# Performance work log

Hardware: AMD Instinct MI355X
Metric: run time of the kernel (lower is better)

Reference implementation:

```python
import jax, jax.numpy as jnp
import numpy as np

EPS = 1e-5

def _bn_train(h, gamma, beta):
    # BatchNorm1d in training mode: batch mean and biased variance over batch dim
    mu = jnp.mean(h, axis=0)
    var = jnp.mean((h - mu) ** 2, axis=0)
    return (h - mu) * jax.lax.rsqrt(var + EPS) * gamma + beta

def setup_inputs() -> dict:
    key = jax.random.key(0)
    ks = jax.random.split(key, 12)
    B, IN, H1, H2, NC = 16384, 4096, 256, 128, 12
    x = jax.random.normal(ks[0], (B, 1, 64, 64), dtype=jnp.float32)
    y = jax.random.randint(ks[1], (B,), 0, NC, dtype=jnp.int32)
    s1 = 1.0 / np.sqrt(IN)
    W1 = jax.random.uniform(ks[2], (H1, IN), jnp.float32, -s1, s1)
    b1 = jax.random.uniform(ks[3], (H1,), jnp.float32, -s1, s1)
    g1 = jax.random.normal(ks[4], (H1,), jnp.float32) * 0.1 + 1.0
    be1 = jax.random.normal(ks[5], (H1,), jnp.float32) * 0.1
    s2 = 1.0 / np.sqrt(H1)
    W2 = jax.random.uniform(ks[6], (H2, H1), jnp.float32, -s2, s2)
    b2 = jax.random.uniform(ks[7], (H2,), jnp.float32, -s2, s2)
    g2 = jax.random.normal(ks[8], (H2,), jnp.float32) * 0.1 + 1.0
    be2 = jax.random.normal(ks[9], (H2,), jnp.float32) * 0.1
    s4 = 1.0 / np.sqrt(H2)
    W4 = jax.random.uniform(ks[10], (NC, H2), jnp.float32, -s4, s4)
    b4 = jax.random.uniform(ks[11], (NC,), jnp.float32, -s4, s4)
    return {"x": x, "W1": W1, "b1": b1, "g1": g1, "be1": be1,
            "W2": W2, "b2": b2, "g2": g2, "be2": be2,
            "W4": W4, "b4": b4, "y": y}

def reference(x, W1, b1, g1, be1, W2, b2, g2, be2, W4, b4, y):
    B = x.shape[0]
    h = x.reshape(B, -1)  # [B, 4096]
    # layer 1: binarized linear + BN(train) + hardtanh (dropout p=0 is identity)
    h = h @ jnp.sign(W1).T + jnp.sign(b1)
    h = jnp.clip(_bn_train(h, g1, be1), -1.0, 1.0)
    # layer 2
    h = h @ jnp.sign(W2).T + jnp.sign(b2)
    h = jnp.clip(_bn_train(h, g2, be2), -1.0, 1.0)
    # final float linear
    return h @ W4.T + b4  # [B, 12]
```

## Files before the change

kernel.cpp:

```cpp
#include <hip/hip_runtime.h>
#include <cstddef>

typedef __attribute__((ext_vector_type(8))) short short8;
typedef __attribute__((ext_vector_type(4))) float f4;
typedef __attribute__((ext_vector_type(4))) unsigned int u4;

__device__ __forceinline__ unsigned int f2bf(float f){
  unsigned int u = __float_as_uint(f);
  u += 0x7fffu + ((u >> 16) & 1u);
  return u >> 16;
}
__device__ __forceinline__ float bflo(unsigned int w){ return __uint_as_float((w & 0xFFFFu) << 16); }
__device__ __forceinline__ float bfhi(unsigned int w){ return __uint_as_float(w & 0xFFFF0000u); }
__device__ __forceinline__ float fsign(float x){ return (x > 0.f) ? 1.f : ((x < 0.f) ? -1.f : 0.f); }
__device__ __forceinline__ float hclip(float x){ return fminf(1.f, fmaxf(-1.f, x)); }

#define BARRIER() do { \
    __builtin_amdgcn_sched_barrier(0); \
    asm volatile("s_waitcnt lgkmcnt(0)" ::: "memory"); \
    __builtin_amdgcn_s_barrier(); \
    asm volatile("" ::: "memory"); \
    __builtin_amdgcn_sched_barrier(0); \
  } while(0)

#define VBAR(N) do { \
    __builtin_amdgcn_sched_barrier(0); \
    asm volatile("s_waitcnt vmcnt(" #N ") lgkmcnt(0)" ::: "memory"); \
    __builtin_amdgcn_s_barrier(); \
    asm volatile("" ::: "memory"); \
    __builtin_amdgcn_sched_barrier(0); \
  } while(0)

#define GL16(gp, lp) __builtin_amdgcn_global_load_lds( \
    (const __attribute__((address_space(1))) void*)(gp), \
    (__attribute__((address_space(3))) void*)(lp), 16, 0, 0)

__global__ void prep_sign_k(const float* __restrict__ W1, unsigned short* __restrict__ w1s,
                            const float* __restrict__ W2, unsigned short* __restrict__ w2s){
  int i = (blockIdx.x * blockDim.x + threadIdx.x) * 8;
  const float* w; unsigned short* o; int off;
  if (i < 1048576){ w = W1; o = w1s; off = i; }
  else            { w = W2; o = w2s; off = i - 1048576; if (off >= 32768) return; }
  f4 a = *(const f4*)(w + off);
  f4 b = *(const f4*)(w + off + 4);
  unsigned short s[8];
  #pragma unroll
  for (int j = 0; j < 4; j++) s[j]   = (a[j] > 0.f) ? 0x3F80u : ((a[j] < 0.f) ? 0xBF80u : 0u);
  #pragma unroll
  for (int j = 0; j < 4; j++) s[4+j] = (b[j] > 0.f) ? 0x3F80u : ((b[j] < 0.f) ? 0xBF80u : 0u);
  u4 v;
  v.x = (unsigned)s[0] | ((unsigned)s[1] << 16);
  v.y = (unsigned)s[2] | ((unsigned)s[3] << 16);
  v.z = (unsigned)s[4] | ((unsigned)s[5] << 16);
  v.w = (unsigned)s[6] | ((unsigned)s[7] << 16);
  *(u4*)(o + off) = v;
}

__global__ __launch_bounds__(512, 1) void gemm1_k(
    const float* __restrict__ x, const unsigned short* __restrict__ w1s,
    const float* __restrict__ b1, unsigned short* __restrict__ h1,
    float* __restrict__ part1s, float* __restrict__ part1q)
{
  __shared__ __align__(16) char lds[147456];
  const int tid  = threadIdx.x;
  const int lane = tid & 63;
  const int wid  = tid >> 6;
  const int wm   = wid >> 2;
  const int wn   = wid & 3;
  const int cl   = lane & 15;
  const int g    = lane >> 4;
  const int row0 = blockIdx.x * 64;

  const int aoff_o = tid * 16;
  const int boff_o = tid * 16;

  f4 acc[2][4];
  const f4 z = {0.f, 0.f, 0.f, 0.f};
  #pragma unroll
  for (int i = 0; i < 2; i++)
    #pragma unroll
    for (int j = 0; j < 4; j++) acc[i][j] = z;

  auto stage = [&](int buf, int kstep){
    char* abuf = lds + buf * 16384;
    char* bbuf = lds + 49152 + buf * 32768;
    #pragma unroll
    for (int c = 0; c < 2; c++){
      int o  = c * 8192 + aoff_o;
      int m  = o >> 8;
      int kb = (o & 255) ^ ((m & 7) << 5);
      const char* src = (const char*)x + (size_t)(row0 + m) * 16384 + kstep * 256 + kb;
      GL16(src, abuf + o);
    }
    #pragma unroll
    for (int c = 0; c < 4; c++){
      int o  = c * 8192 + boff_o;
      int n  = o >> 7;
      int kb = (o & 127) ^ ((n & 7) << 4);
      const char* src = (const char*)w1s + (size_t)n * 8192 + kstep * 128 + kb;
      GL16(src, bbuf + o);
    }
  };

  auto compute = [&](int buf){
    const char* abuf = lds + buf * 16384;
    const char* bbuf = lds + 49152 + buf * 32768;
    short8 bf[4][2];
    #pragma unroll
    for (int fn = 0; fn < 4; fn++){
      int n = wn * 64 + fn * 16 + cl;
      #pragma unroll
      for (int ks = 0; ks < 2; ks++){
        int off = (n * 128 + ks * 64 + g * 16) ^ ((n & 7) << 4);
        bf[fn][ks] = *(const short8*)(bbuf + off);
      }
    }
    short8 af[2][2];
    #pragma unroll
    for (int fm = 0; fm < 2; fm++){
      int m = wm * 32 + fm * 16 + cl;
      #pragma unroll
      for (int ks = 0; ks < 2; ks++){
        int off = (m * 256 + ks * 128 + g * 32) ^ ((m & 7) << 5);
        f4 lo = *(const f4*)(abuf + off);
        f4 hi = *(const f4*)(abuf + off + 16);
        u4 pk;
        pk.x = f2bf(lo[0]) | (f2bf(lo[1]) << 16);
        pk.y = f2bf(lo[2]) | (f2bf(lo[3]) << 16);
        pk.z = f2bf(hi[0]) | (f2bf(hi[1]) << 16);
        pk.w = f2bf(hi[2]) | (f2bf(hi[3]) << 16);
        af[fm][ks] = *(short8*)&pk;
      }
    }
    #pragma unroll
    for (int ks = 0; ks < 2; ks++)
      #pragma unroll
      for (int fm = 0; fm < 2; fm++)
        #pragma unroll
        for (int fn = 0; fn < 4; fn++)
          acc[fm][fn] = __builtin_amdgcn_mfma_f32_16x16x32_bf16(af[fm][ks], bf[fn][ks], acc[fm][fn], 0, 0, 0);
  };

  stage(0, 0);
  stage(1, 1);
  VBAR(6);
  int cb = 0;
  for (int k = 0; k < 64; ++k){
    int sb = cb + 2; if (sb >= 3) sb -= 3;
    if (k < 62) stage(sb, k + 2);
    compute(cb);
    if (k < 62)      VBAR(6);
    else if (k < 63) VBAR(0);
    cb = (cb == 2) ? 0 : cb + 1;
  }

  #pragma unroll
  for (int fn = 0; fn < 4; fn++){
    int c = wn * 64 + fn * 16 + cl;
    float sb = fsign(b1[c]);
    float s = 0.f, q = 0.f;
    #pragma unroll
    for (int fm = 0; fm < 2; fm++){
      int rbase = row0 + wm * 32 + fm * 16 + g * 4;
      #pragma unroll
      for (int i = 0; i < 4; i++){
        float v = acc[fm][fn][i] + sb;
        h1[(size_t)(rbase + i) * 256 + c] = (unsigned short)f2bf(v);
        s += v; q += v * v;
      }
    }
    s += __shfl_xor(s, 16, 64); s += __shfl_xor(s, 32, 64);
    q += __shfl_xor(q, 16, 64); q += __shfl_xor(q, 32, 64);
    if (g == 0){
      part1s[c * 512 + blockIdx.x * 2 + wm] = s;
      part1q[c * 512 + blockIdx.x * 2 + wm] = q;
    }
  }
}

template<int COLS, int NBLK>
__global__ __launch_bounds__(64) void params_k(
    const float* __restrict__ ps, const float* __restrict__ pq,
    const float* __restrict__ g, const float* __restrict__ be,
    float* __restrict__ ab){
  int j = blockIdx.x * 64 + threadIdx.x;
  const f4* vs = (const f4*)(ps + (size_t)j * NBLK);
  const f4* vq = (const f4*)(pq + (size_t)j * NBLK);
  f4 s4 = {0,0,0,0}, q4 = {0,0,0,0};
  #pragma unroll 8
  for (int b = 0; b < NBLK/4; b++){ s4 += vs[b]; q4 += vq[b]; }
  float s = s4[0]+s4[1]+s4[2]+s4[3];
  float q = q4[0]+q4[1]+q4[2]+q4[3];
  float mu  = s * (1.f/16384.f);
  float var = q * (1.f/16384.f) - mu*mu;
  float a   = g[j] * rsqrtf(var + 1e-5f);
  ab[j] = a;
  ab[COLS + j] = be[j] - mu*a;
}

__global__ __launch_bounds__(512) void gemm2_k(
    const unsigned short* __restrict__ h1, const unsigned short* __restrict__ w2s,
    const float* __restrict__ b2, const float* __restrict__ ab1,
    unsigned short* __restrict__ h2, float* __restrict__ part2s, float* __restrict__ part2q)
{
  __shared__ __align__(16) char lds[32768];
  __shared__ __align__(16) float a1l[256];
  __shared__ __align__(16) float c1l[256];
  const int tid  = threadIdx.x;
  const int lane = tid & 63;
  const int wid  = tid >> 6;
  const int cl   = lane & 15;
  const int g    = lane >> 4;
  const int klo  = g * 8;
  const int row0 = blockIdx.x * 64;

  if (tid < 256) a1l[tid] = ab1[tid];
  else           c1l[tid - 256] = ab1[tid];

  const int am  = tid >> 3;
  const int ak0 = (tid & 7) * 8;
  const unsigned short* hA = h1 + (size_t)(row0 + am) * 256 + ak0;
  const int aw = ((am * 128) + (ak0 * 2)) ^ ((am & 7) << 4);
  const unsigned short* wbase = w2s + (size_t)(wid * 16 + cl) * 256 + klo;

  u4 q0 = *(const u4*)(hA);
  u4 q1 = *(const u4*)(hA + 64);
  u4 q2 = *(const u4*)(hA + 128);
  u4 q3 = *(const u4*)(hA + 192);
  short8 Bq0, Bq1, Br0, Br1;
  Bq0 = *(const short8*)(wbase);
  Bq1 = *(const short8*)(wbase + 32);

  BARRIER();

#define TRW(KB, RAW) do { \
    f4 _a0 = *(const f4*)(&a1l[(KB)*64 + ak0]); \
    f4 _a1 = *(const f4*)(&a1l[(KB)*64 + ak0 + 4]); \
    f4 _c0 = *(const f4*)(&c1l[(KB)*64 + ak0]); \
    f4 _c1 = *(const f4*)(&c1l[(KB)*64 + ak0 + 4]); \
    float _t0 = hclip(_a0[0]*bflo(RAW.x) + _c0[0]); \
    float _t1 = hclip(_a0[1]*bfhi(RAW.x) + _c0[1]); \
    float _t2 = hclip(_a0[2]*bflo(RAW.y) + _c0[2]); \
    float _t3 = hclip(_a0[3]*bfhi(RAW.y) + _c0[3]); \
    float _t4 = hclip(_a1[0]*bflo(RAW.z) + _c1[0]); \
    float _t5 = hclip(_a1[1]*bfhi(RAW.z) + _c1[1]); \
    float _t6 = hclip(_a1[2]*bflo(RAW.w) + _c1[2]); \
    float _t7 = hclip(_a1[3]*bfhi(RAW.w) + _c1[3]); \
    u4 _v; \
    _v.x = f2bf(_t0) | (f2bf(_t1) << 16); \
    _v.y = f2bf(_t2) | (f2bf(_t3) << 16); \
    _v.z = f2bf(_t4) | (f2bf(_t5) << 16); \
    _v.w = f2bf(_t6) | (f2bf(_t7) << 16); \
    *(u4*)(lds + (KB)*8192 + aw) = _v; \
  } while(0)

  TRW(0, q0); TRW(1, q1); TRW(2, q2); TRW(3, q3);
#undef TRW
  BARRIER();

  f4 acc[4];
  const f4 z = {0.f, 0.f, 0.f, 0.f};
  #pragma unroll
  for (int i = 0; i < 4; i++) acc[i] = z;

#define LOADB2(P, KB) do { \
    B##P##0 = *(const short8*)(wbase + (KB)*64); \
    B##P##1 = *(const short8*)(wbase + (KB)*64 + 32); \
  } while(0)

#define COMP2(BASE, P) do { \
    const char* _ab = (const char*)(BASE); \
    short8 _af[4][2]; \
    _Pragma("unroll") \
    for (int fm = 0; fm < 4; fm++){ \
      int _m = fm*16 + cl; \
      _af[fm][0] = *(const short8*)(_ab + ((_m*128 + klo*2) ^ ((_m & 7) << 4))); \
      _af[fm][1] = *(const short8*)(_ab + ((_m*128 + (32 + klo)*2) ^ ((_m & 7) << 4))); \
    } \
    _Pragma("unroll") \
    for (int fm = 0; fm < 4; fm++){ \
      acc[fm] = __builtin_amdgcn_mfma_f32_16x16x32_bf16(_af[fm][0], B##P##0, acc[fm], 0, 0, 0); \
      acc[fm] = __builtin_amdgcn_mfma_f32_16x16x32_bf16(_af[fm][1], B##P##1, acc[fm], 0, 0, 0); \
    } \
  } while(0)

  LOADB2(r, 1);
  COMP2(lds,         q);
  LOADB2(q, 2);
  COMP2(lds +  8192, r);
  LOADB2(r, 3);
  COMP2(lds + 16384, q);
  COMP2(lds + 24576, r);
#undef COMP2
#undef LOADB2

  {
    int c = wid*16 + cl;
    float sb = fsign(b2[c]);
    float s = 0.f, q = 0.f;
    #pragma unroll
    for (int fm = 0; fm < 4; fm++){
      int rbase = row0 + fm*16 + g*4;
      #pragma unroll
      for (int i = 0; i < 4; i++){
        float v = acc[fm][i] + sb;
        h2[(size_t)(rbase + i)*128 + c] = (unsigned short)f2bf(v);
        s += v; q += v*v;
      }
    }
    s += __shfl_xor(s, 16, 64); s += __shfl_xor(s, 32, 64);
    q += __shfl_xor(q, 16, 64); q += __shfl_xor(q, 32, 64);
    if (g == 0){
      part2s[c*256 + blockIdx.x] = s;
      part2q[c*256 + blockIdx.x] = q;
    }
  }
}

__global__ __launch_bounds__(128) void final_k(
    const unsigned short* __restrict__ h2,
    const float* __restrict__ part2s, const float* __restrict__ part2q,
    const float* __restrict__ g2, const float* __restrict__ be2,
    const float* __restrict__ W4, const float* __restrict__ b4,
    float* __restrict__ out)
{
  __shared__ __align__(16) float W4l[12*128];
  __shared__ __align__(16) float a2l[128];
  __shared__ __align__(16) float c2l[128];
  const int t = threadIdx.x;
  #pragma unroll
  for (int i = 0; i < 3; i++)
    *(f4*)&W4l[(i*128 + t)*4] = *(const f4*)(W4 + (i*128 + t)*4);
  {
    const f4* vs = (const f4*)(part2s + t*256);
    const f4* vq = (const f4*)(part2q + t*256);
    f4 s4 = {0,0,0,0}, q4 = {0,0,0,0};
    #pragma unroll 8
    for (int b = 0; b < 64; b++){ s4 += vs[b]; q4 += vq[b]; }
    float s = s4[0]+s4[1]+s4[2]+s4[3];
    float q = q4[0]+q4[1]+q4[2]+q4[3];
    float mu  = s * (1.f/16384.f);
    float var = q * (1.f/16384.f) - mu*mu;
    float a   = g2[t] * rsqrtf(var + 1e-5f);
    a2l[t] = a;
    c2l[t] = be2[t] - mu*a;
  }
  __syncthreads();

  const int r = blockIdx.x * 128 + t;
  const u4* hp = (const u4*)(h2 + (size_t)r * 128);
  u4 hv0 = hp[0], hv1 = hp[1], hv2 = hp[2],  hv3 = hp[3];
  u4 hv4 = hp[4], hv5 = hp[5], hv6 = hp[6],  hv7 = hp[7];
  u4 hv8 = hp[8], hv9 = hp[9], hv10 = hp[10], hv11 = hp[11];
  u4 hv12 = hp[12], hv13 = hp[13], hv14 = hp[14], hv15 = hp[15];

  float acc[12];
  #pragma unroll
  for (int o = 0; o < 12; o++) acc[o] = b4[o];

#define FPROC(HV, J) do { \
    f4 a0 = *(const f4*)&a2l[(J)*8];     f4 a1 = *(const f4*)&a2l[(J)*8 + 4]; \
    f4 c0 = *(const f4*)&c2l[(J)*8];     f4 c1 = *(const f4*)&c2l[(J)*8 + 4]; \
    float tt0 = hclip(a0[0]*bflo(HV.x) + c0[0]); \
    float tt1 = hclip(a0[1]*bfhi(HV.x) + c0[1]); \
    float tt2 = hclip(a0[2]*bflo(HV.y) + c0[2]); \
    float tt3 = hclip(a0[3]*bfhi(HV.y) + c0[3]); \
    float tt4 = hclip(a1[0]*bflo(HV.z) + c1[0]); \
    float tt5 = hclip(a1[1]*bfhi(HV.z) + c1[1]); \
    float tt6 = hclip(a1[2]*bflo(HV.w) + c1[2]); \
    float tt7 = hclip(a1[3]*bfhi(HV.w) + c1[3]); \
    _Pragma("unroll") \
    for (int o = 0; o < 12; o++){ \
      f4 w0 = *(const f4*)&W4l[o*128 + (J)*8]; \
      f4 w1 = *(const f4*)&W4l[o*128 + (J)*8 + 4]; \
      acc[o] += tt0*w0[0] + tt1*w0[1] + tt2*w0[2] + tt3*w0[3] \
              + tt4*w1[0] + tt5*w1[1] + tt6*w1[2] + tt7*w1[3]; \
    } \
  } while(0)

  FPROC(hv0, 0);  FPROC(hv1, 1);  FPROC(hv2, 2);   FPROC(hv3, 3);
  FPROC(hv4, 4);  FPROC(hv5, 5);  FPROC(hv6, 6);   FPROC(hv7, 7);
  FPROC(hv8, 8);  FPROC(hv9, 9);  FPROC(hv10, 10); FPROC(hv11, 11);
  FPROC(hv12, 12); FPROC(hv13, 13); FPROC(hv14, 14); FPROC(hv15, 15);
#undef FPROC

  #pragma unroll
  for (int o = 0; o < 12; o++) out[(size_t)r*12 + o] = acc[o];
}

extern "C" void kernel_launch(void* const* d_in, const int* in_sizes, int n_in,
                              void* d_out, int out_size, void* d_ws, size_t ws_size,
                              hipStream_t stream)
{
  const float* x   = (const float*)d_in[0];
  const float* W1  = (const float*)d_in[1];
  const float* b1  = (const float*)d_in[2];
  const float* g1  = (const float*)d_in[3];
  const float* be1 = (const float*)d_in[4];
  const float* W2  = (const float*)d_in[5];
  const float* b2  = (const float*)d_in[6];
  const float* g2  = (const float*)d_in[7];
  const float* be2 = (const float*)d_in[8];
  const float* W4  = (const float*)d_in[9];
  const float* b4  = (const float*)d_in[10];
  float* out = (float*)d_out;

  char* ws = (char*)d_ws;
  unsigned short* h1     = (unsigned short*)(ws);
  unsigned short* h2     = (unsigned short*)(ws + 8388608);
  unsigned short* w1s    = (unsigned short*)(ws + 12582912);
  unsigned short* w2s    = (unsigned short*)(ws + 14680064);
  float*          part1s = (float*)(ws + 14745600);
  float*          part1q = (float*)(ws + 15269888);
  float*          part2s = (float*)(ws + 15794176);
  float*          part2q = (float*)(ws + 15925248);
  float*          ab1    = (float*)(ws + 16056320);

  prep_sign_k<<<528, 256, 0, stream>>>(W1, w1s, W2, w2s);
  gemm1_k<<<256, 512, 0, stream>>>(x, w1s, b1, h1, part1s, part1q);
  params_k<256, 512><<<4, 64, 0, stream>>>(part1s, part1q, g1, be1, ab1);
  gemm2_k<<<256, 512, 0, stream>>>(h1, w2s, b2, ab1, h2, part2s, part2q);
  final_k<<<128, 128, 0, stream>>>(h2, part2s, part2q, g2, be2, W4, b4, out);
}
```

Before: 120.6 us.

## Load x tiles into registers and store bf16-packed A to LDS

The A operand (fp32 x) used to go global→LDS via direct loads, and was converted to bf16 at every MFMA fragment read. Now each thread loads its x slice into registers three steps ahead, packs it to bf16 once, and writes it to a double-buffered bf16 LDS tile. The B operand moves to a 4-deep LDS ring. This halves A's LDS footprint and read traffic and removes the redundant conversions. In exchange it needs more registers to hold in-flight A data and a manually unrolled, three-phase pipeline with tighter vmcnt waits.

```diff
diff --git a/kernel.cpp b/kernel.cpp
--- a/kernel.cpp
+++ b/kernel.cpp
@@ -71,7 +71,11 @@
   const int g    = lane >> 4;
   const int row0 = blockIdx.x * 64;
 
-  const int aoff_o = tid * 16;
+  const int am  = tid >> 3;
+  const int ak0 = (tid & 7) * 8;
+  const float* xA = x + (size_t)(row0 + am) * 4096 + ak0;
+  const int aw = (am * 128 + ak0 * 2) ^ ((am & 7) << 4);
+
   const int boff_o = tid * 16;
 
   f4 acc[2][4];
@@ -81,78 +85,90 @@
     #pragma unroll
     for (int j = 0; j < 4; j++) acc[i][j] = z;
 
-  auto stage = [&](int buf, int kstep){
-    char* abuf = lds + buf * 16384;
-    char* bbuf = lds + 49152 + buf * 32768;
-    #pragma unroll
-    for (int c = 0; c < 2; c++){
-      int o  = c * 8192 + aoff_o;
-      int m  = o >> 8;
-      int kb = (o & 255) ^ ((m & 7) << 5);
-      const char* src = (const char*)x + (size_t)(row0 + m) * 16384 + kstep * 256 + kb;
-      GL16(src, abuf + o);
-    }
-    #pragma unroll
-    for (int c = 0; c < 4; c++){
-      int o  = c * 8192 + boff_o;
-      int n  = o >> 7;
-      int kb = (o & 127) ^ ((n & 7) << 4);
-      const char* src = (const char*)w1s + (size_t)n * 8192 + kstep * 128 + kb;
-      GL16(src, bbuf + o);
-    }
-  };
-
-  auto compute = [&](int buf){
-    const char* abuf = lds + buf * 16384;
-    const char* bbuf = lds + 49152 + buf * 32768;
-    short8 bf[4][2];
-    #pragma unroll
-    for (int fn = 0; fn < 4; fn++){
-      int n = wn * 64 + fn * 16 + cl;
-      #pragma unroll
-      for (int ks = 0; ks < 2; ks++){
-        int off = (n * 128 + ks * 64 + g * 16) ^ ((n & 7) << 4);
-        bf[fn][ks] = *(const short8*)(bbuf + off);
-      }
-    }
-    short8 af[2][2];
-    #pragma unroll
-    for (int fm = 0; fm < 2; fm++){
-      int m = wm * 32 + fm * 16 + cl;
-      #pragma unroll
-      for (int ks = 0; ks < 2; ks++){
-        int off = (m * 256 + ks * 128 + g * 32) ^ ((m & 7) << 5);
-        f4 lo = *(const f4*)(abuf + off);
-        f4 hi = *(const f4*)(abuf + off + 16);
-        u4 pk;
-        pk.x = f2bf(lo[0]) | (f2bf(lo[1]) << 16);
-        pk.y = f2bf(lo[2]) | (f2bf(lo[3]) << 16);
-        pk.z = f2bf(hi[0]) | (f2bf(hi[1]) << 16);
-        pk.w = f2bf(hi[2]) | (f2bf(hi[3]) << 16);
-        af[fm][ks] = *(short8*)&pk;
-      }
-    }
-    #pragma unroll
-    for (int ks = 0; ks < 2; ks++)
-      #pragma unroll
-      for (int fm = 0; fm < 2; fm++)
-        #pragma unroll
-        for (int fn = 0; fn < 4; fn++)
-          acc[fm][fn] = __builtin_amdgcn_mfma_f32_16x16x32_bf16(af[fm][ks], bf[fn][ks], acc[fm][fn], 0, 0, 0);
-  };
-
-  stage(0, 0);
-  stage(1, 1);
-  VBAR(6);
-  int cb = 0;
-  for (int k = 0; k < 64; ++k){
-    int sb = cb + 2; if (sb >= 3) sb -= 3;
-    if (k < 62) stage(sb, k + 2);
-    compute(cb);
-    if (k < 62)      VBAR(6);
-    else if (k < 63) VBAR(0);
-    cb = (cb == 2) ? 0 : cb + 1;
+  f4 rA0_0, rA0_1, rA1_0, rA1_1, rA2_0, rA2_1;
+
+#define ISSUEA(S, KB) do { \
+    rA##S##_0 = *(const f4*)(xA + (KB)*64); \
+    rA##S##_1 = *(const f4*)(xA + (KB)*64 + 4); \
+  } while(0)
+
+#define ISSUEB(BSLOT, KB) do { \
+    char* _dst = lds + 16384 + (BSLOT)*32768; \
+    _Pragma("unroll") \
+    for (int c = 0; c < 4; c++){ \
+      int _o  = c*8192 + boff_o; \
+      int _n  = _o >> 7; \
+      int _kb = (_o & 127) ^ ((_n & 7) << 4); \
+      GL16((const char*)w1s + (size_t)_n*8192 + (size_t)(KB)*128 + _kb, _dst + _o); \
+    } } while(0)
+
+#define PACKA(S, ABUF) do { \
+    u4 _v; \
+    _v.x = f2bf(rA##S##_0[0]) | (f2bf(rA##S##_0[1]) << 16); \
+    _v.y = f2bf(rA##S##_0[2]) | (f2bf(rA##S##_0[3]) << 16); \
+    _v.z = f2bf(rA##S##_1[0]) | (f2bf(rA##S##_1[1]) << 16); \
+    _v.w = f2bf(rA##S##_1[2]) | (f2bf(rA##S##_1[3]) << 16); \
+    *(u4*)(lds + (ABUF)*8192 + aw) = _v; \
+  } while(0)
+
+#define COMPUTE(ABASE, BBASE) do { \
+    const char* _ab = (const char*)(ABASE); \
+    const char* _bb = (const char*)(BBASE); \
+    short8 _af[2][2]; short8 _bf[4][2]; \
+    _Pragma("unroll") \
+    for (int fm = 0; fm < 2; fm++){ \
+      int _m = wm*32 + fm*16 + cl; \
+      _Pragma("unroll") \
+      for (int ks = 0; ks < 2; ks++) \
+        _af[fm][ks] = *(const short8*)(_ab + ((_m*128 + ks*64 + g*16) ^ ((_m & 7) << 4))); \
+    } \
+    _Pragma("unroll") \
+    for (int fn = 0; fn < 4; fn++){ \
+      int _n = wn*64 + fn*16 + cl; \
+      _Pragma("unroll") \
+      for (int ks = 0; ks < 2; ks++) \
+        _bf[fn][ks] = *(const short8*)(_bb + ((_n*128 + ks*64 + g*16) ^ ((_n & 7) << 4))); \
+    } \
+    _Pragma("unroll") \
+    for (int ks = 0; ks < 2; ks++) \
+      _Pragma("unroll") \
+      for (int fm = 0; fm < 2; fm++) \
+        _Pragma("unroll") \
+        for (int fn = 0; fn < 4; fn++) \
+          acc[fm][fn] = __builtin_amdgcn_mfma_f32_16x16x32_bf16(_af[fm][ks], _bf[fn][ks], acc[fm][fn], 0, 0, 0); \
+  } while(0)
+
+#define STEP(K, SI, SP) do { \
+    const int _k3 = (K) + 3; \
+    const int _kc = (_k3 > 63) ? 63 : _k3; \
+    ISSUEA(SI, _kc); \
+    ISSUEB(_k3 & 3, _kc); \
+    __builtin_amdgcn_sched_barrier(0); \
+    COMPUTE(lds + ((K) & 1) * 8192, lds + 16384 + ((K) & 3) * 32768); \
+    __builtin_amdgcn_sched_barrier(0); \
+    PACKA(SP, ((K) + 1) & 1); \
+    VBAR(12); \
+  } while(0)
+
+  ISSUEA(0, 0); ISSUEB(0, 0);
+  ISSUEA(1, 1); ISSUEB(1, 1);
+  ISSUEA(2, 2); ISSUEB(2, 2);
+  PACKA(0, 0);
+  VBAR(12);
+
+  for (int kk = 0; kk < 63; kk += 3){
+    STEP(kk,     0, 1);
+    STEP(kk + 1, 1, 2);
+    STEP(kk + 2, 2, 0);
   }
+  COMPUTE(lds + 8192, lds + 16384 + 3 * 32768);
+  asm volatile("s_waitcnt vmcnt(0)" ::: "memory");
+
+#undef STEP
+#undef COMPUTE
+#undef PACKA
+#undef ISSUEB
+#undef ISSUEA
 
   #pragma unroll
   for (int fn = 0; fn < 4; fn++){
```

New measurement: 121.1 us. About the same (+0.4%).
